# Kernel tuning notes

Measured on AMD Instinct MI355X. Metric: run time of the kernel, lower is better.

Reference implementation:

```python
import jax, jax.numpy as jnp
import numpy as np

VOCAB, E, S, H, L = 32000, 1024, 2048, 16, 2
HS = E // H  # head_size = 64
EPS = 1e-5


def setup_inputs() -> dict:
    key = jax.random.key(0)
    ks = jax.random.split(key, 12)
    sc = 0.02
    inp = {
        "seq": jax.random.randint(ks[0], (S,), 0, VOCAB, dtype=jnp.int64)
        if jax.config.jax_enable_x64 else jax.random.randint(ks[0], (S,), 0, VOCAB, dtype=jnp.int32),
        "tok_emb": jax.random.normal(ks[1], (VOCAB, E), jnp.float32) * sc,
        "pos_emb": jax.random.normal(ks[2], (S, E), jnp.float32) * sc,
        "Wq": jax.random.normal(ks[3], (L, H, E, HS), jnp.float32) * sc,
        "Wk": jax.random.normal(ks[4], (L, H, E, HS), jnp.float32) * sc,
        "Wv": jax.random.normal(ks[5], (L, H, E, HS), jnp.float32) * sc,
        "Wr": jax.random.normal(ks[6], (L, E, E), jnp.float32) * sc,
        "br": jnp.zeros((L, E), jnp.float32),
        "W1": jax.random.normal(ks[7], (L, E, 4 * E), jnp.float32) * sc,
        "b1": jnp.zeros((L, 4 * E), jnp.float32),
        "W2": jax.random.normal(ks[8], (L, 4 * E, E), jnp.float32) * sc,
        "b2": jnp.zeros((L, E), jnp.float32),
        "ln_g": jnp.ones((L, E), jnp.float32),
        "ln_b": jnp.zeros((L, E), jnp.float32),
    }
    return inp


def _layer_norm(x, g, b):
    mu = jnp.mean(x, axis=-1, keepdims=True)
    var = jnp.mean(jnp.square(x - mu), axis=-1, keepdims=True)
    return (x - mu) * jax.lax.rsqrt(var + EPS) * g + b


def reference(seq, tok_emb, pos_emb, Wq, Wk, Wv, Wr, br, W1, b1, W2, b2, ln_g, ln_b):
    # embeddings: [S, E]
    x = tok_emb[seq] + pos_emb
    att_maps = []
    for l in range(L):
        # NOTE: the torch Block reuses the SAME LayerNorm instance twice per block.
        x = _layer_norm(x, ln_g[l], ln_b[l])
        # per-head projections: [H, S, HS]
        q = jnp.einsum('se,hed->hsd', x, Wq[l])
        k = jnp.einsum('se,hed->hsd', x, Wk[l])
        v = jnp.einsum('se,hed->hsd', x, Wv[l])
        # unmasked (encoder) attention, full [H, S, S] scores
        atts = jax.nn.softmax(jnp.einsum('hsd,htd->hst', q, k) / np.sqrt(HS), axis=-1)
        av = jnp.einsum('hst,htd->hsd', atts, v)  # [H, S, HS]
        cat = jnp.transpose(av, (1, 0, 2)).reshape(S, H * HS)  # concat heads -> [S, E]
        x = x + cat @ Wr[l] + br[l]
        x = _layer_norm(x, ln_g[l], ln_b[l])
        x = x + jax.nn.relu(x @ W1[l] + b1[l]) @ W2[l] + b2[l]
        att_maps.append(atts)
    return x, jnp.stack(att_maps)  # ([S,E], [L,H,S,S])
```

## Files before the change

### kernel.cpp

```cpp
#include <hip/hip_runtime.h>
#include <hip/hip_bf16.h>


constexpr int S_ = 2048;
constexpr int E_ = 1024;
constexpr int H_ = 16;
constexpr int HS_ = 64;
constexpr int L_ = 2;
constexpr int FF_ = 4096;

typedef __bf16 bf16;
typedef __bf16 bf16x8 __attribute__((ext_vector_type(8)));
typedef __bf16 bf16x4 __attribute__((ext_vector_type(4)));
typedef float f32x4 __attribute__((ext_vector_type(4)));

__device__ __forceinline__ void gld16(const void* g, const void* l) {
  __builtin_amdgcn_global_load_lds(
      (const __attribute__((address_space(1))) unsigned int*)g,
      (__attribute__((address_space(3))) unsigned int*)l, 16, 0, 0);
}

__global__ __launch_bounds__(256) void embed_ln_k(const int* __restrict__ seq,
                                                  const float* __restrict__ tok,
                                                  const float* __restrict__ pos,
                                                  const float* __restrict__ gw,
                                                  const float* __restrict__ bw,
                                                  float* __restrict__ x,
                                                  bf16* __restrict__ xb) {
  __shared__ float red[8];
  const int row = blockIdx.x, tid = threadIdx.x;
  const int t = seq[row];
  float4 v = ((const float4*)(tok + (long)t * E_))[tid];
  float4 p = ((const float4*)(pos + (long)row * E_))[tid];
  v.x += p.x; v.y += p.y; v.z += p.z; v.w += p.w;
  float s = v.x + v.y + v.z + v.w;
  float ss = v.x * v.x + v.y * v.y + v.z * v.z + v.w * v.w;
  for (int off = 32; off; off >>= 1) {
    s += __shfl_down(s, off);
    ss += __shfl_down(ss, off);
  }
  if ((tid & 63) == 0) { red[(tid >> 6) * 2] = s; red[(tid >> 6) * 2 + 1] = ss; }
  __syncthreads();
  if (tid == 0) {
    float S0 = 0, SS = 0;
    for (int i = 0; i < 4; ++i) { S0 += red[i * 2]; SS += red[i * 2 + 1]; }
    red[0] = S0; red[1] = SS;
  }
  __syncthreads();
  const float mu = red[0] * (1.f / E_);
  const float var = red[1] * (1.f / E_) - mu * mu;
  const float rs = rsqrtf(var + 1e-5f);
  float4 gv = ((const float4*)gw)[tid], bv = ((const float4*)bw)[tid];
  float4 o;
  o.x = (v.x - mu) * rs * gv.x + bv.x;
  o.y = (v.y - mu) * rs * gv.y + bv.y;
  o.z = (v.z - mu) * rs * gv.z + bv.z;
  o.w = (v.w - mu) * rs * gv.w + bv.w;
  ((float4*)(x + (long)row * E_))[tid] = o;
  bf16x4 ob;
  ob[0] = (__bf16)o.x; ob[1] = (__bf16)o.y; ob[2] = (__bf16)o.z; ob[3] = (__bf16)o.w;
  ((bf16x4*)(xb + (long)row * E_))[tid] = ob;
}

__global__ __launch_bounds__(256) void layernorm_k(float* __restrict__ x,
                                                   const float* __restrict__ gw,
                                                   const float* __restrict__ bw,
                                                   bf16* __restrict__ xb) {
  __shared__ float red[8];
  const int row = blockIdx.x, tid = threadIdx.x;
  float4 v = ((const float4*)(x + (long)row * E_))[tid];
  float s = v.x + v.y + v.z + v.w;
  float ss = v.x * v.x + v.y * v.y + v.z * v.z + v.w * v.w;
  for (int off = 32; off; off >>= 1) {
    s += __shfl_down(s, off);
    ss += __shfl_down(ss, off);
  }
  if ((tid & 63) == 0) { red[(tid >> 6) * 2] = s; red[(tid >> 6) * 2 + 1] = ss; }
  __syncthreads();
  if (tid == 0) {
    float S0 = 0, SS = 0;
    for (int i = 0; i < 4; ++i) { S0 += red[i * 2]; SS += red[i * 2 + 1]; }
    red[0] = S0; red[1] = SS;
  }
  __syncthreads();
  const float mu = red[0] * (1.f / E_);
  const float var = red[1] * (1.f / E_) - mu * mu;
  const float rs = rsqrtf(var + 1e-5f);
  float4 gv = ((const float4*)gw)[tid], bv = ((const float4*)bw)[tid];
  float4 o;
  o.x = (v.x - mu) * rs * gv.x + bv.x;
  o.y = (v.y - mu) * rs * gv.y + bv.y;
  o.z = (v.z - mu) * rs * gv.z + bv.z;
  o.w = (v.w - mu) * rs * gv.w + bv.w;
  ((float4*)(x + (long)row * E_))[tid] = o;
  bf16x4 ob;
  ob[0] = (__bf16)o.x; ob[1] = (__bf16)o.y; ob[2] = (__bf16)o.z; ob[3] = (__bf16)o.w;
  ((bf16x4*)(xb + (long)row * E_))[tid] = ob;
}

__global__ __launch_bounds__(256) void repack_k(const float* __restrict__ wq,
                                                const float* __restrict__ wk,
                                                const float* __restrict__ wv,
                                                const float* __restrict__ wr,
                                                const float* __restrict__ w1,
                                                const float* __restrict__ w2,
                                                bf16* __restrict__ qkvT,
                                                bf16* __restrict__ wrT,
                                                bf16* __restrict__ w1T,
                                                bf16* __restrict__ w2T) {
  __shared__ float t[32][33];
  const int tx = threadIdx.x, ty = threadIdx.y;
  const int bid = blockIdx.x;
  const float* src;
  bf16* dst;
  long ld_in, ld_out, r0, c0;
  if (bid < 3072) {
    const int j = bid >> 10;
    const int z = (bid & 1023) >> 6;
    const int rem = bid & 63;
    r0 = (rem >> 1) * 32;
    c0 = (rem & 1) * 32;
    const float* w = j == 0 ? wq : (j == 1 ? wk : wv);
    src = w + (long)z * E_ * HS_;
    dst = qkvT + (long)j * E_ * E_ + (long)z * HS_ * E_;
    ld_in = HS_; ld_out = E_;
  } else if (bid < 4096) {
    const int idx = bid - 3072;
    r0 = (idx >> 5) * 32; c0 = (idx & 31) * 32;
    src = wr; dst = wrT; ld_in = E_; ld_out = E_;
  } else if (bid < 8192) {
    const int idx = bid - 4096;
    r0 = (idx >> 7) * 32; c0 = (idx & 127) * 32;
    src = w1; dst = w1T; ld_in = FF_; ld_out = E_;
  } else {
    const int idx = bid - 8192;
    r0 = (idx >> 5) * 32; c0 = (idx & 31) * 32;
    src = w2; dst = w2T; ld_in = E_; ld_out = FF_;
  }
#pragma unroll
  for (int i = 0; i < 4; ++i)
    t[ty + 8 * i][tx] = src[(r0 + ty + 8 * i) * ld_in + c0 + tx];
  __syncthreads();
#pragma unroll
  for (int i = 0; i < 4; ++i)
    dst[(c0 + ty + 8 * i) * ld_out + r0 + tx] = (__bf16)t[tx][ty + 8 * i];
}

__global__ __launch_bounds__(256) void trans_b2b(const bf16* __restrict__ in,
                                                 bf16* __restrict__ out,
                                                 long ld_in, long ld_out) {
  __shared__ bf16 t[32][33];
  const int tx = threadIdx.x, ty = threadIdx.y;
  const long r0 = (long)blockIdx.x * 32, c0 = (long)blockIdx.y * 32;
#pragma unroll
  for (int i = 0; i < 4; ++i)
    t[ty + 8 * i][tx] = in[(r0 + ty + 8 * i) * ld_in + c0 + tx];
  __syncthreads();
#pragma unroll
  for (int i = 0; i < 4; ++i)
    out[(c0 + ty + 8 * i) * ld_out + r0 + tx] = t[tx][ty + 8 * i];
}

template <int WM, int WN>
__global__ __launch_bounds__(WM * WN * 64) void gemm_lds(
    const bf16* __restrict__ A, const bf16* __restrict__ B,
    long lda, long ldb, int K, int mtiles, float scale,
    const float* __restrict__ bias, const float* __restrict__ resid, int relu,
    float* __restrict__ Cf, long ldc, bf16* __restrict__ Cb, long ldcb) {
  constexpr int BM = WM * 64, BN = WN * 64, NW = WM * WN;
  constexpr int ABYTES = BM * 64;
  constexpr int BUFB = ABYTES + BN * 64;
  constexpr int NCH = BUFB / 1024;
  constexpr int CPT = NCH / NW;
  static_assert(CPT == 4 || CPT == 6, "unexpected CPT");
  __shared__ char smem[3 * BUFB];

  const int tid = threadIdx.x, wid = tid >> 6, lane = tid & 63;
  const int cpx = gridDim.x >> 3;
  const int bid = blockIdx.x;
  const int wg = (bid & 7) * cpx + (bid >> 3);
  const long m0 = (long)(wg % mtiles) * BM;
  const long n0 = (long)(wg / mtiles) * BN;

  const char* gsrc[CPT];
  int ldsbase[CPT];
#pragma unroll
  for (int i = 0; i < CPT; ++i) {
    const int c = wid + i * NW;
    const int s = c * 1024 + lane * 16;
    const bf16* base;
    int kb;
    if (s < ABYTES) {
      const int row = s >> 6;
      kb = (s ^ ((row & 3) << 4)) & 63;
      base = A + (m0 + row) * lda;
    } else {
      const int s2 = s - ABYTES;
      const int row = s2 >> 6;
      kb = (s2 ^ ((row & 3) << 4)) & 63;
      base = B + (n0 + row) * ldb;
    }
    gsrc[i] = (const char*)base + kb;
    ldsbase[i] = c * 1024;
  }

  const int fr = lane & 15, fg = lane >> 4;
  const int wm = wid % WM, wn = wid / WM;
  int aoff[4], boff[4];
#pragma unroll
  for (int t = 0; t < 4; ++t) {
    const int m = wm * 64 + t * 16 + fr;
    aoff[t] = m * 64 + ((16 * fg) ^ ((m & 3) << 4));
    const int n = wn * 64 + t * 16 + fr;
    boff[t] = ABYTES + n * 64 + ((16 * fg) ^ ((n & 3) << 4));
  }

  f32x4 acc[4][4];
#pragma unroll
  for (int i = 0; i < 4; ++i)
#pragma unroll
    for (int j = 0; j < 4; ++j) acc[i][j] = (f32x4){0.f, 0.f, 0.f, 0.f};

  const int nt = K >> 5;

  auto stage = [&](int tile, int buf) {
    const long koff = (long)tile * 64;
#pragma unroll
    for (int i = 0; i < CPT; ++i)
      gld16(gsrc[i] + koff, smem + buf * BUFB + ldsbase[i]);
  };

  stage(0, 0);
  stage(1, 1);

  int cur = 0;
  for (int t = 0; t < nt; ++t) {
    if (t < nt - 1) {
      if constexpr (CPT == 4) asm volatile("s_waitcnt vmcnt(4)" ::: "memory");
      else asm volatile("s_waitcnt vmcnt(6)" ::: "memory");
    } else {
      asm volatile("s_waitcnt vmcnt(0)" ::: "memory");
    }
    __builtin_amdgcn_s_barrier();
    if (t + 2 < nt) {
      int sb = cur + 2; if (sb >= 3) sb -= 3;
      stage(t + 2, sb);
    }
    const char* sbuf = smem + cur * BUFB;
    bf16x8 a[4], b[4];
#pragma unroll
    for (int i = 0; i < 4; ++i) a[i] = *(const bf16x8*)(sbuf + aoff[i]);
#pragma unroll
    for (int i = 0; i < 4; ++i) b[i] = *(const bf16x8*)(sbuf + boff[i]);
#pragma unroll
    for (int i = 0; i < 4; ++i)
#pragma unroll
      for (int j = 0; j < 4; ++j)
        acc[i][j] = __builtin_amdgcn_mfma_f32_16x16x32_bf16(a[i], b[j], acc[i][j], 0, 0, 0);
    cur = cur + 1; if (cur >= 3) cur -= 3;
  }

#pragma unroll
  for (int tm = 0; tm < 4; ++tm) {
#pragma unroll
    for (int tn = 0; tn < 4; ++tn) {
      const long col = n0 + wn * 64 + tn * 16 + fr;
#pragma unroll
      for (int i = 0; i < 4; ++i) {
        const long row = m0 + wm * 64 + tm * 16 + fg * 4 + i;
        float v = acc[tm][tn][i] * scale;
        if (bias) v += bias[col];
        if (relu) v = v > 0.f ? v : 0.f;
        if (resid) v += resid[row * ldc + col];
        if (Cf) Cf[row * ldc + col] = v;
        if (Cb) Cb[row * ldcb + col] = (__bf16)v;
      }
    }
  }
}

__global__ __launch_bounds__(256, 2) void gemm_ksplit(
    const bf16* __restrict__ A, const bf16* __restrict__ B,
    long lda, long ldb, int K, int mtiles, float scale,
    const float* __restrict__ bias, const float* __restrict__ resid, int relu,
    float* __restrict__ Cf, long ldc, bf16* __restrict__ Cb, long ldcb) {
  __shared__ char smem[4 * 16384];

  const int tid = threadIdx.x, w = tid >> 6, lane = tid & 63;
  const int cpx = gridDim.x >> 3;
  const int bid = blockIdx.x;
  const int wg = (bid & 7) * cpx + (bid >> 3);
  const long m0 = (long)(wg % mtiles) * 64;
  const long n0 = (long)(wg / mtiles) * 64;
  const int Kq = K >> 2;
  const long k0w = (long)w * Kq;

  const char* gsrc[8];
  int ldsoff[8];
#pragma unroll
  for (int i = 0; i < 8; ++i) {
    const int s = (i & 3) * 1024 + lane * 16;
    const int row = s >> 6;
    const int kb = (s ^ ((row & 3) << 4)) & 63;
    const bf16* base = (i < 4) ? (A + (m0 + row) * lda + k0w)
                               : (B + (n0 + row) * ldb + k0w);
    gsrc[i] = (const char*)base + kb;
    ldsoff[i] = w * 16384 + i * 1024;
  }

  const int fr = lane & 15, fg = lane >> 4;
  int aoff[4], boff[4];
#pragma unroll
  for (int t = 0; t < 4; ++t) {
    const int m = t * 16 + fr;
    aoff[t] = w * 16384 + m * 64 + ((16 * fg) ^ ((m & 3) << 4));
    boff[t] = aoff[t] + 4096;
  }

  f32x4 acc[4][4];
#pragma unroll
  for (int i = 0; i < 4; ++i)
#pragma unroll
    for (int j = 0; j < 4; ++j) acc[i][j] = (f32x4){0.f, 0.f, 0.f, 0.f};

  const int nt = Kq >> 5;

  auto stage = [&](int tile, int buf) {
    const long koff = (long)tile * 64;
#pragma unroll
    for (int i = 0; i < 8; ++i)
      gld16(gsrc[i] + koff, smem + ldsoff[i] + buf * 8192);
  };

  stage(0, 0);
  if (nt > 1) stage(1, 1);

  for (int t = 0; t < nt; ++t) {
    if (t + 1 < nt) asm volatile("s_waitcnt vmcnt(8)" ::: "memory");
    else asm volatile("s_waitcnt vmcnt(0)" ::: "memory");
    const int bsel = (t & 1) * 8192;
    bf16x8 a[4], b[4];
#pragma unroll
    for (int i = 0; i < 4; ++i) a[i] = *(const bf16x8*)(smem + aoff[i] + bsel);
#pragma unroll
    for (int i = 0; i < 4; ++i) b[i] = *(const bf16x8*)(smem + boff[i] + bsel);
    __builtin_amdgcn_s_setprio(1);
#pragma unroll
    for (int i = 0; i < 4; ++i)
#pragma unroll
      for (int j = 0; j < 4; ++j)
        acc[i][j] = __builtin_amdgcn_mfma_f32_16x16x32_bf16(a[i], b[j], acc[i][j], 0, 0, 0);
    __builtin_amdgcn_s_setprio(0);
    if (t + 2 < nt) stage(t + 2, t & 1);
  }

  __syncthreads();
#pragma unroll
  for (int f = 0; f < 16; ++f)
    *(f32x4*)(smem + w * 16384 + f * 1024 + lane * 16) = acc[f >> 2][f & 3];
  __syncthreads();

#pragma unroll
  for (int tn = 0; tn < 4; ++tn) {
    const int f = w * 4 + tn;
    f32x4 v0 = *(const f32x4*)(smem + 0 * 16384 + f * 1024 + lane * 16);
    f32x4 v1 = *(const f32x4*)(smem + 1 * 16384 + f * 1024 + lane * 16);
    f32x4 v2 = *(const f32x4*)(smem + 2 * 16384 + f * 1024 + lane * 16);
    f32x4 v3 = *(const f32x4*)(smem + 3 * 16384 + f * 1024 + lane * 16);
    f32x4 sv;
#pragma unroll
    for (int i = 0; i < 4; ++i) sv[i] = v0[i] + v1[i] + v2[i] + v3[i];
    const long col = n0 + tn * 16 + fr;
#pragma unroll
    for (int i = 0; i < 4; ++i) {
      const long row = m0 + w * 16 + fg * 4 + i;
      float v = sv[i] * scale;
      if (bias) v += bias[col];
      if (relu) v = v > 0.f ? v : 0.f;
      if (resid) v += resid[row * ldc + col];
      if (Cf) Cf[row * ldc + col] = v;
      if (Cb) Cb[row * ldcb + col] = (__bf16)v;
    }
  }
}

__global__ __launch_bounds__(256, 2) void attn_fused(
    const bf16* __restrict__ qkv,
    const bf16* __restrict__ vt,
    float* __restrict__ att,
    bf16* __restrict__ avb) {
  constexpr int QB = 64, KB = 128;
  constexpr int NKT = S_ / KB;
  constexpr float C2 = 0.1803368801111244f;
  __shared__ char plds[QB * 256];

  const int tid = threadIdx.x, lane = tid & 63, w = tid >> 6;
  const int fr = lane & 15, fg = lane >> 4;
  const int bid = blockIdx.x;
  const int wg = (bid & 7) * 64 + (bid >> 3);
  const int h = wg >> 5;
  const long q0 = (long)(wg & 31) * QB;
  const int q = w * 16 + fr;
  const int swz = (q & 15) << 4;

  bf16x8 qf[2];
#pragma unroll
  for (int k0 = 0; k0 < 2; ++k0)
    qf[k0] = *(const bf16x8*)(qkv + (q0 + q) * (3 * E_) + h * HS_ + k0 * 32 + fg * 8);

  float l_ = 0.f;

  for (int kt = 0; kt < NKT; ++kt) {
    const long t0 = (long)kt * KB;
    bf16x8 kf[8][2];
#pragma unroll
    for (int mt = 0; mt < 8; ++mt)
#pragma unroll
      for (int k0 = 0; k0 < 2; ++k0)
        kf[mt][k0] = *(const bf16x8*)(qkv + (t0 + mt * 16 + fr) * (3 * E_) +
                                      E_ + h * HS_ + k0 * 32 + fg * 8);
    f32x4 acc[8];
#pragma unroll
    for (int mt = 0; mt < 8; ++mt) acc[mt] = (f32x4){0.f, 0.f, 0.f, 0.f};
    __builtin_amdgcn_s_setprio(1);
#pragma unroll
    for (int k0 = 0; k0 < 2; ++k0)
#pragma unroll
      for (int mt = 0; mt < 8; ++mt)
        acc[mt] = __builtin_amdgcn_mfma_f32_16x16x32_bf16(kf[mt][k0], qf[k0], acc[mt], 0, 0, 0);
    __builtin_amdgcn_s_setprio(0);
    float sum = 0.f;
#pragma unroll
    for (int mt = 0; mt < 8; ++mt)
#pragma unroll
      for (int i = 0; i < 4; ++i) sum += __builtin_amdgcn_exp2f(acc[mt][i] * C2);
    l_ += sum;
  }
  l_ += __shfl_xor(l_, 16);
  l_ += __shfl_xor(l_, 32);
  const float li = -__log2f(l_);

  f32x4 ao[4];
#pragma unroll
  for (int d = 0; d < 4; ++d) ao[d] = (f32x4){0.f, 0.f, 0.f, 0.f};

  for (int kt = 0; kt < NKT; ++kt) {
    const long t0 = (long)kt * KB;
    bf16x8 kf[8][2];
#pragma unroll
    for (int mt = 0; mt < 8; ++mt)
#pragma unroll
      for (int k0 = 0; k0 < 2; ++k0)
        kf[mt][k0] = *(const bf16x8*)(qkv + (t0 + mt * 16 + fr) * (3 * E_) +
                                      E_ + h * HS_ + k0 * 32 + fg * 8);
    f32x4 acc[8];
#pragma unroll
    for (int mt = 0; mt < 8; ++mt) acc[mt] = (f32x4){0.f, 0.f, 0.f, 0.f};
    __builtin_amdgcn_s_setprio(1);
#pragma unroll
    for (int k0 = 0; k0 < 2; ++k0)
#pragma unroll
      for (int mt = 0; mt < 8; ++mt)
        acc[mt] = __builtin_amdgcn_mfma_f32_16x16x32_bf16(kf[mt][k0], qf[k0], acc[mt], 0, 0, 0);
    __builtin_amdgcn_s_setprio(0);

    float* arow = att + ((long)h * S_ + q0 + q) * S_ + t0;
#pragma unroll
    for (int mt = 0; mt < 8; ++mt) {
      f32x4 pv;
#pragma unroll
      for (int i = 0; i < 4; ++i)
        pv[i] = __builtin_amdgcn_exp2f(fmaf(acc[mt][i], C2, li));
      __builtin_nontemporal_store(pv, (f32x4*)(arow + mt * 16 + fg * 4));
      bf16x4 pb;
      pb[0] = (__bf16)pv[0]; pb[1] = (__bf16)pv[1];
      pb[2] = (__bf16)pv[2]; pb[3] = (__bf16)pv[3];
      const int tb = (mt * 16 + fg * 4) * 2;
      *(bf16x4*)(plds + q * 256 + ((tb & ~15) ^ swz) + (tb & 15)) = pb;
    }

#pragma unroll
    for (int k0 = 0; k0 < 4; ++k0) {
      const bf16x8 bq = *(const bf16x8*)(plds + q * 256 + ((k0 * 64 + fg * 16) ^ swz));
      __builtin_amdgcn_s_setprio(1);
#pragma unroll
      for (int dmt = 0; dmt < 4; ++dmt) {
        bf16x8 av = *(const bf16x8*)(vt + (long)(h * HS_ + dmt * 16 + fr) * S_ +
                                     t0 + k0 * 32 + fg * 8);
        ao[dmt] = __builtin_amdgcn_mfma_f32_16x16x32_bf16(av, bq, ao[dmt], 0, 0, 0);
      }
      __builtin_amdgcn_s_setprio(0);
    }
  }

#pragma unroll
  for (int dmt = 0; dmt < 4; ++dmt) {
    bf16x4 o;
    o[0] = (__bf16)ao[dmt][0]; o[1] = (__bf16)ao[dmt][1];
    o[2] = (__bf16)ao[dmt][2]; o[3] = (__bf16)ao[dmt][3];
    *(bf16x4*)(avb + (q0 + q) * E_ + h * HS_ + dmt * 16 + fg * 4) = o;
  }
}

extern "C" void kernel_launch(void* const* d_in, const int* in_sizes, int n_in,
                              void* d_out, int out_size, void* d_ws, size_t ws_size,
                              hipStream_t stream) {
  const int* seq = (const int*)d_in[0];
  const float* tok_emb = (const float*)d_in[1];
  const float* pos_emb = (const float*)d_in[2];
  const float* Wq = (const float*)d_in[3];
  const float* Wk = (const float*)d_in[4];
  const float* Wv = (const float*)d_in[5];
  const float* Wr = (const float*)d_in[6];
  const float* br = (const float*)d_in[7];
  const float* W1 = (const float*)d_in[8];
  const float* b1 = (const float*)d_in[9];
  const float* W2 = (const float*)d_in[10];
  const float* b2 = (const float*)d_in[11];
  const float* ln_g = (const float*)d_in[12];
  const float* ln_b = (const float*)d_in[13];

  float* outx = (float*)d_out;
  float* att_all = outx + (long)S_ * E_;

  char* w = (char*)d_ws;
  auto alloc = [&](size_t bytes) {
    char* p = w;
    w += (bytes + 255) & ~(size_t)255;
    return p;
  };
  float* x = (float*)alloc((size_t)S_ * E_ * 4);
  bf16* xb = (bf16*)alloc((size_t)S_ * E_ * 2);
  bf16* qkvb = (bf16*)alloc((size_t)S_ * 3 * E_ * 2);
  bf16* vt = (bf16*)alloc((size_t)E_ * S_ * 2);
  bf16* avb = (bf16*)alloc((size_t)S_ * E_ * 2);
  bf16* hb = (bf16*)alloc((size_t)S_ * FF_ * 2);
  bf16* wqkvT = (bf16*)alloc((size_t)3 * E_ * E_ * 2);
  bf16* wrT = (bf16*)alloc((size_t)E_ * E_ * 2);
  bf16* w1T = (bf16*)alloc((size_t)E_ * FF_ * 2);
  bf16* w2T = (bf16*)alloc((size_t)E_ * FF_ * 2);
  (void)ws_size; (void)in_sizes; (void)n_in; (void)out_size;

  embed_ln_k<<<S_, 256, 0, stream>>>(seq, tok_emb, pos_emb, ln_g, ln_b, x, xb);

  for (int l = 0; l < L_; ++l) {
    repack_k<<<12288, dim3(32, 8, 1), 0, stream>>>(
        Wq + (long)l * H_ * E_ * HS_, Wk + (long)l * H_ * E_ * HS_,
        Wv + (long)l * H_ * E_ * HS_, Wr + (long)l * E_ * E_,
        W1 + (long)l * E_ * FF_, W2 + (long)l * FF_ * E_,
        wqkvT, wrT, w1T, w2T);

    if (l > 0)
      layernorm_k<<<S_, 256, 0, stream>>>(x, ln_g + (long)l * E_, ln_b + (long)l * E_, xb);

    gemm_lds<1, 2><<<768, 128, 0, stream>>>(
        xb, wqkvT, E_, E_, E_, 32, 1.f, nullptr, nullptr, 0,
        nullptr, 0, qkvb, 3 * E_);

    trans_b2b<<<dim3(S_ / 32, E_ / 32, 1), dim3(32, 8, 1), 0, stream>>>(
        qkvb + 2 * E_, vt, 3 * E_, S_);

    float* att_l = att_all + (long)l * H_ * S_ * S_;
    attn_fused<<<512, 256, 0, stream>>>(qkvb, vt, att_l, avb);

    gemm_ksplit<<<32 * 16, 256, 0, stream>>>(
        avb, wrT, E_, E_, E_, 32, 1.f, br + (long)l * E_, x, 0,
        x, E_, nullptr, 0);

    layernorm_k<<<S_, 256, 0, stream>>>(x, ln_g + (long)l * E_, ln_b + (long)l * E_, xb);

    gemm_lds<2, 2><<<dim3(16 * 32), 256, 0, stream>>>(
        xb, w1T, E_, E_, E_, 16, 1.f, b1 + (long)l * FF_, nullptr, 1,
        nullptr, 0, hb, FF_);

    float* xdst = (l == L_ - 1) ? outx : x;
    gemm_ksplit<<<32 * 16, 256, 0, stream>>>(
        hb, w2T, FF_, FF_, FF_, 32, 1.f, b2 + (long)l * E_, x, 0,
        xdst, E_, nullptr, 0);
  }
}
```

Baseline: 691.8 us.

## Fuse V transpose into QKV GEMM epilogue and retile FFN1 GEMM

The QKV projection GEMM now writes the V columns directly into a transposed layout. It stages each output tile through swizzled LDS and stores contiguous rows, which removes the separate trans_b2b kernel launch and its extra read and write of V. V tiles no longer write to qkvb, and the attention kernel only reads V from vt. The FFN1 GEMM also switches from 128x128 tiles with 512 blocks to 64x128 tiles with 1024 blocks of 128 threads, giving more blocks at the cost of less reuse per tile.

```diff
diff --git a/kernel.cpp b/kernel.cpp
--- a/kernel.cpp
+++ b/kernel.cpp
@@ -146,27 +146,13 @@
     dst[(c0 + ty + 8 * i) * ld_out + r0 + tx] = (__bf16)t[tx][ty + 8 * i];
 }
 
-__global__ __launch_bounds__(256) void trans_b2b(const bf16* __restrict__ in,
-                                                 bf16* __restrict__ out,
-                                                 long ld_in, long ld_out) {
-  __shared__ bf16 t[32][33];
-  const int tx = threadIdx.x, ty = threadIdx.y;
-  const long r0 = (long)blockIdx.x * 32, c0 = (long)blockIdx.y * 32;
-#pragma unroll
-  for (int i = 0; i < 4; ++i)
-    t[ty + 8 * i][tx] = in[(r0 + ty + 8 * i) * ld_in + c0 + tx];
-  __syncthreads();
-#pragma unroll
-  for (int i = 0; i < 4; ++i)
-    out[(c0 + ty + 8 * i) * ld_out + r0 + tx] = t[tx][ty + 8 * i];
-}
-
 template <int WM, int WN>
 __global__ __launch_bounds__(WM * WN * 64) void gemm_lds(
     const bf16* __restrict__ A, const bf16* __restrict__ B,
     long lda, long ldb, int K, int mtiles, float scale,
     const float* __restrict__ bias, const float* __restrict__ resid, int relu,
-    float* __restrict__ Cf, long ldc, bf16* __restrict__ Cb, long ldcb) {
+    float* __restrict__ Cf, long ldc, bf16* __restrict__ Cb, long ldcb,
+    bf16* __restrict__ Vt, long vthresh) {
   constexpr int BM = WM * 64, BN = WN * 64, NW = WM * WN;
   constexpr int ABYTES = BM * 64;
   constexpr int BUFB = ABYTES + BN * 64;
@@ -258,6 +244,34 @@
       for (int j = 0; j < 4; ++j)
         acc[i][j] = __builtin_amdgcn_mfma_f32_16x16x32_bf16(a[i], b[j], acc[i][j], 0, 0, 0);
     cur = cur + 1; if (cur >= 3) cur -= 3;
+  }
+
+  if (Vt && n0 >= vthresh) {
+    static_assert(BN * BM * 2 <= 3 * BUFB, "LDS too small for V transpose");
+    __syncthreads();
+#pragma unroll
+    for (int tm = 0; tm < 4; ++tm) {
+#pragma unroll
+      for (int tn = 0; tn < 4; ++tn) {
+        const int col = wn * 64 + tn * 16 + fr;
+        const int rowb = wm * 64 + tm * 16 + fg * 4;
+        bf16x4 o;
+#pragma unroll
+        for (int i = 0; i < 4; ++i) o[i] = (__bf16)(acc[tm][tn][i] * scale);
+        *(bf16x4*)(smem + col * (BM * 2) + ((rowb * 2) ^ ((col & 7) << 4))) = o;
+      }
+    }
+    __syncthreads();
+    constexpr int CHUNKS = BM * 2 / 16;
+    constexpr int COLS_PER_REP = (NW * 64) / CHUNKS;
+    const int k = tid % CHUNKS;
+#pragma unroll
+    for (int rep = 0; rep < BN / COLS_PER_REP; ++rep) {
+      const int col = (tid / CHUNKS) + rep * COLS_PER_REP;
+      bf16x8 v = *(const bf16x8*)(smem + col * (BM * 2) + ((k * 16) ^ ((col & 7) << 4)));
+      *(bf16x8*)(Vt + (n0 - vthresh + col) * (long)S_ + m0 + k * 8) = v;
+    }
+    return;
   }
 
 #pragma unroll
@@ -555,10 +569,7 @@
 
     gemm_lds<1, 2><<<768, 128, 0, stream>>>(
         xb, wqkvT, E_, E_, E_, 32, 1.f, nullptr, nullptr, 0,
-        nullptr, 0, qkvb, 3 * E_);
-
-    trans_b2b<<<dim3(S_ / 32, E_ / 32, 1), dim3(32, 8, 1), 0, stream>>>(
-        qkvb + 2 * E_, vt, 3 * E_, S_);
+        nullptr, 0, qkvb, 3 * E_, vt, 2 * E_);
 
     float* att_l = att_all + (long)l * H_ * S_ * S_;
     attn_fused<<<512, 256, 0, stream>>>(qkvb, vt, att_l, avb);
@@ -569,9 +580,9 @@
 
     layernorm_k<<<S_, 256, 0, stream>>>(x, ln_g + (long)l * E_, ln_b + (long)l * E_, xb);
 
-    gemm_lds<2, 2><<<dim3(16 * 32), 256, 0, stream>>>(
-        xb, w1T, E_, E_, E_, 16, 1.f, b1 + (long)l * FF_, nullptr, 1,
-        nullptr, 0, hb, FF_);
+    gemm_lds<1, 2><<<1024, 128, 0, stream>>>(
+        xb, w1T, E_, E_, E_, 32, 1.f, b1 + (long)l * FF_, nullptr, 1,
+        nullptr, 0, hb, FF_, nullptr, 0x7fffffffL);
 
     float* xdst = (l == L_ - 1) ? outx : x;
     gemm_ksplit<<<32 * 16, 256, 0, stream>>>(
```

Measured after the change: 700.1 us. About the same (+1.2%).

## Overlap weight repacking with embedding and attention kernels via merged grids

Applied to the files above, without the earlier changes.

Merges the layer-0 weight repack into the embedding+LayerNorm launch, and the layer-1 repack into the layer-0 attention launch as extra blocks. A second weight buffer set is used when workspace allows, so layer-1 weights can be converted while layer-0 attention runs. The aim is to hide the memory-bound repack traffic behind other work and drop separate launches. The cost is extra workspace, and attn_repack_k loses the (256,2) launch-bounds hint, which could change register allocation for the attention blocks.

```diff
diff --git a/kernel.cpp b/kernel.cpp
--- a/kernel.cpp
+++ b/kernel.cpp
@@ -20,97 +20,19 @@
       (__attribute__((address_space(3))) unsigned int*)l, 16, 0, 0);
 }
 
-__global__ __launch_bounds__(256) void embed_ln_k(const int* __restrict__ seq,
-                                                  const float* __restrict__ tok,
-                                                  const float* __restrict__ pos,
-                                                  const float* __restrict__ gw,
-                                                  const float* __restrict__ bw,
-                                                  float* __restrict__ x,
-                                                  bf16* __restrict__ xb) {
-  __shared__ float red[8];
-  const int row = blockIdx.x, tid = threadIdx.x;
-  const int t = seq[row];
-  float4 v = ((const float4*)(tok + (long)t * E_))[tid];
-  float4 p = ((const float4*)(pos + (long)row * E_))[tid];
-  v.x += p.x; v.y += p.y; v.z += p.z; v.w += p.w;
-  float s = v.x + v.y + v.z + v.w;
-  float ss = v.x * v.x + v.y * v.y + v.z * v.z + v.w * v.w;
-  for (int off = 32; off; off >>= 1) {
-    s += __shfl_down(s, off);
-    ss += __shfl_down(ss, off);
-  }
-  if ((tid & 63) == 0) { red[(tid >> 6) * 2] = s; red[(tid >> 6) * 2 + 1] = ss; }
-  __syncthreads();
-  if (tid == 0) {
-    float S0 = 0, SS = 0;
-    for (int i = 0; i < 4; ++i) { S0 += red[i * 2]; SS += red[i * 2 + 1]; }
-    red[0] = S0; red[1] = SS;
-  }
-  __syncthreads();
-  const float mu = red[0] * (1.f / E_);
-  const float var = red[1] * (1.f / E_) - mu * mu;
-  const float rs = rsqrtf(var + 1e-5f);
-  float4 gv = ((const float4*)gw)[tid], bv = ((const float4*)bw)[tid];
-  float4 o;
-  o.x = (v.x - mu) * rs * gv.x + bv.x;
-  o.y = (v.y - mu) * rs * gv.y + bv.y;
-  o.z = (v.z - mu) * rs * gv.z + bv.z;
-  o.w = (v.w - mu) * rs * gv.w + bv.w;
-  ((float4*)(x + (long)row * E_))[tid] = o;
-  bf16x4 ob;
-  ob[0] = (__bf16)o.x; ob[1] = (__bf16)o.y; ob[2] = (__bf16)o.z; ob[3] = (__bf16)o.w;
-  ((bf16x4*)(xb + (long)row * E_))[tid] = ob;
-}
-
-__global__ __launch_bounds__(256) void layernorm_k(float* __restrict__ x,
-                                                   const float* __restrict__ gw,
-                                                   const float* __restrict__ bw,
-                                                   bf16* __restrict__ xb) {
-  __shared__ float red[8];
-  const int row = blockIdx.x, tid = threadIdx.x;
-  float4 v = ((const float4*)(x + (long)row * E_))[tid];
-  float s = v.x + v.y + v.z + v.w;
-  float ss = v.x * v.x + v.y * v.y + v.z * v.z + v.w * v.w;
-  for (int off = 32; off; off >>= 1) {
-    s += __shfl_down(s, off);
-    ss += __shfl_down(ss, off);
-  }
-  if ((tid & 63) == 0) { red[(tid >> 6) * 2] = s; red[(tid >> 6) * 2 + 1] = ss; }
-  __syncthreads();
-  if (tid == 0) {
-    float S0 = 0, SS = 0;
-    for (int i = 0; i < 4; ++i) { S0 += red[i * 2]; SS += red[i * 2 + 1]; }
-    red[0] = S0; red[1] = SS;
-  }
-  __syncthreads();
-  const float mu = red[0] * (1.f / E_);
-  const float var = red[1] * (1.f / E_) - mu * mu;
-  const float rs = rsqrtf(var + 1e-5f);
-  float4 gv = ((const float4*)gw)[tid], bv = ((const float4*)bw)[tid];
-  float4 o;
-  o.x = (v.x - mu) * rs * gv.x + bv.x;
-  o.y = (v.y - mu) * rs * gv.y + bv.y;
-  o.z = (v.z - mu) * rs * gv.z + bv.z;
-  o.w = (v.w - mu) * rs * gv.w + bv.w;
-  ((float4*)(x + (long)row * E_))[tid] = o;
-  bf16x4 ob;
-  ob[0] = (__bf16)o.x; ob[1] = (__bf16)o.y; ob[2] = (__bf16)o.z; ob[3] = (__bf16)o.w;
-  ((bf16x4*)(xb + (long)row * E_))[tid] = ob;
-}
-
-__global__ __launch_bounds__(256) void repack_k(const float* __restrict__ wq,
-                                                const float* __restrict__ wk,
-                                                const float* __restrict__ wv,
-                                                const float* __restrict__ wr,
-                                                const float* __restrict__ w1,
-                                                const float* __restrict__ w2,
-                                                bf16* __restrict__ qkvT,
-                                                bf16* __restrict__ wrT,
-                                                bf16* __restrict__ w1T,
-                                                bf16* __restrict__ w2T) {
-  __shared__ float t[32][33];
-  const int tx = threadIdx.x, ty = threadIdx.y;
-  const int bid = blockIdx.x;
+__device__ __forceinline__ void repack_tile(int bid, int tid,
+                                            const float* __restrict__ wq,
+                                            const float* __restrict__ wk,
+                                            const float* __restrict__ wv,
+                                            const float* __restrict__ wr,
+                                            const float* __restrict__ w1,
+                                            const float* __restrict__ w2,
+                                            bf16* __restrict__ qkvT,
+                                            bf16* __restrict__ wrT,
+                                            bf16* __restrict__ w1T,
+                                            bf16* __restrict__ w2T,
+                                            float (*t)[33]) {
+  const int tx = tid & 31, ty = tid >> 5;
   const float* src;
   bf16* dst;
   long ld_in, ld_out, r0, c0;
@@ -146,6 +68,101 @@
     dst[(c0 + ty + 8 * i) * ld_out + r0 + tx] = (__bf16)t[tx][ty + 8 * i];
 }
 
+__global__ __launch_bounds__(256) void embed_ln_repack_k(
+    const int* __restrict__ seq, const float* __restrict__ tok,
+    const float* __restrict__ pos, const float* __restrict__ gw,
+    const float* __restrict__ bw, float* __restrict__ x, bf16* __restrict__ xb,
+    const float* wq, const float* wk, const float* wv, const float* wr,
+    const float* w1, const float* w2,
+    bf16* qkvT, bf16* wrT, bf16* w1T, bf16* w2T) {
+  __shared__ float red[8];
+  __shared__ float t[32][33];
+  const int tid = threadIdx.x;
+  if (blockIdx.x >= S_) {
+    repack_tile(blockIdx.x - S_, tid, wq, wk, wv, wr, w1, w2,
+                qkvT, wrT, w1T, w2T, t);
+    return;
+  }
+  const int row = blockIdx.x;
+  const int tk = seq[row];
+  float4 v = ((const float4*)(tok + (long)tk * E_))[tid];
+  float4 p = ((const float4*)(pos + (long)row * E_))[tid];
+  v.x += p.x; v.y += p.y; v.z += p.z; v.w += p.w;
+  float s = v.x + v.y + v.z + v.w;
+  float ss = v.x * v.x + v.y * v.y + v.z * v.z + v.w * v.w;
+  for (int off = 32; off; off >>= 1) {
+    s += __shfl_down(s, off);
+    ss += __shfl_down(ss, off);
+  }
+  if ((tid & 63) == 0) { red[(tid >> 6) * 2] = s; red[(tid >> 6) * 2 + 1] = ss; }
+  __syncthreads();
+  if (tid == 0) {
+    float S0 = 0, SS = 0;
+    for (int i = 0; i < 4; ++i) { S0 += red[i * 2]; SS += red[i * 2 + 1]; }
+    red[0] = S0; red[1] = SS;
+  }
+  __syncthreads();
+  const float mu = red[0] * (1.f / E_);
+  const float var = red[1] * (1.f / E_) - mu * mu;
+  const float rs = rsqrtf(var + 1e-5f);
+  float4 gv = ((const float4*)gw)[tid], bv = ((const float4*)bw)[tid];
+  float4 o;
+  o.x = (v.x - mu) * rs * gv.x + bv.x;
+  o.y = (v.y - mu) * rs * gv.y + bv.y;
+  o.z = (v.z - mu) * rs * gv.z + bv.z;
+  o.w = (v.w - mu) * rs * gv.w + bv.w;
+  ((float4*)(x + (long)row * E_))[tid] = o;
+  bf16x4 ob;
+  ob[0] = (__bf16)o.x; ob[1] = (__bf16)o.y; ob[2] = (__bf16)o.z; ob[3] = (__bf16)o.w;
+  ((bf16x4*)(xb + (long)row * E_))[tid] = ob;
+}
+
+__global__ __launch_bounds__(256) void layernorm_k(float* __restrict__ x,
+                                                   const float* __restrict__ gw,
+                                                   const float* __restrict__ bw,
+                                                   bf16* __restrict__ xb) {
+  __shared__ float red[8];
+  const int row = blockIdx.x, tid = threadIdx.x;
+  float4 v = ((const float4*)(x + (long)row * E_))[tid];
+  float s = v.x + v.y + v.z + v.w;
+  float ss = v.x * v.x + v.y * v.y + v.z * v.z + v.w * v.w;
+  for (int off = 32; off; off >>= 1) {
+    s += __shfl_down(s, off);
+    ss += __shfl_down(ss, off);
+  }
+  if ((tid & 63) == 0) { red[(tid >> 6) * 2] = s; red[(tid >> 6) * 2 + 1] = ss; }
+  __syncthreads();
+  if (tid == 0) {
+    float S0 = 0, SS = 0;
+    for (int i = 0; i < 4; ++i) { S0 += red[i * 2]; SS += red[i * 2 + 1]; }
+    red[0] = S0; red[1] = SS;
+  }
+  __syncthreads();
+  const float mu = red[0] * (1.f / E_);
+  const float var = red[1] * (1.f / E_) - mu * mu;
+  const float rs = rsqrtf(var + 1e-5f);
+  float4 gv = ((const float4*)gw)[tid], bv = ((const float4*)bw)[tid];
+  float4 o;
+  o.x = (v.x - mu) * rs * gv.x + bv.x;
+  o.y = (v.y - mu) * rs * gv.y + bv.y;
+  o.z = (v.z - mu) * rs * gv.z + bv.z;
+  o.w = (v.w - mu) * rs * gv.w + bv.w;
+  ((float4*)(x + (long)row * E_))[tid] = o;
+  bf16x4 ob;
+  ob[0] = (__bf16)o.x; ob[1] = (__bf16)o.y; ob[2] = (__bf16)o.z; ob[3] = (__bf16)o.w;
+  ((bf16x4*)(xb + (long)row * E_))[tid] = ob;
+}
+
+__global__ __launch_bounds__(256) void repack_k(const float* wq, const float* wk,
+                                                const float* wv, const float* wr,
+                                                const float* w1, const float* w2,
+                                                bf16* qkvT, bf16* wrT,
+                                                bf16* w1T, bf16* w2T) {
+  __shared__ float t[32][33];
+  repack_tile(blockIdx.x, threadIdx.x, wq, wk, wv, wr, w1, w2,
+              qkvT, wrT, w1T, w2T, t);
+}
+
 __global__ __launch_bounds__(256) void trans_b2b(const bf16* __restrict__ in,
                                                  bf16* __restrict__ out,
                                                  long ld_in, long ld_out) {
@@ -384,22 +401,20 @@
   }
 }
 
-__global__ __launch_bounds__(256, 2) void attn_fused(
-    const bf16* __restrict__ qkv,
-    const bf16* __restrict__ vt,
-    float* __restrict__ att,
-    bf16* __restrict__ avb) {
-  constexpr int QB = 64, KB = 128;
+__device__ __forceinline__ void attn_body(int bid, int tid,
+                                          const bf16* __restrict__ qkv,
+                                          const bf16* __restrict__ vt,
+                                          float* __restrict__ att,
+                                          bf16* __restrict__ avb,
+                                          char* plds) {
+  constexpr int KB = 128;
   constexpr int NKT = S_ / KB;
   constexpr float C2 = 0.1803368801111244f;
-  __shared__ char plds[QB * 256];
-
-  const int tid = threadIdx.x, lane = tid & 63, w = tid >> 6;
+  const int lane = tid & 63, w = tid >> 6;
   const int fr = lane & 15, fg = lane >> 4;
-  const int bid = blockIdx.x;
   const int wg = (bid & 7) * 64 + (bid >> 3);
   const int h = wg >> 5;
-  const long q0 = (long)(wg & 31) * QB;
+  const long q0 = (long)(wg & 31) * 64;
   const int q = w * 16 + fr;
   const int swz = (q & 15) << 4;
 
@@ -499,6 +514,29 @@
     o[0] = (__bf16)ao[dmt][0]; o[1] = (__bf16)ao[dmt][1];
     o[2] = (__bf16)ao[dmt][2]; o[3] = (__bf16)ao[dmt][3];
     *(bf16x4*)(avb + (q0 + q) * E_ + h * HS_ + dmt * 16 + fg * 4) = o;
+  }
+}
+
+__global__ __launch_bounds__(256, 2) void attn_fused(
+    const bf16* __restrict__ qkv, const bf16* __restrict__ vt,
+    float* __restrict__ att, bf16* __restrict__ avb) {
+  __shared__ char plds[64 * 256];
+  attn_body(blockIdx.x, threadIdx.x, qkv, vt, att, avb, plds);
+}
+
+__global__ __launch_bounds__(256) void attn_repack_k(
+    const bf16* __restrict__ qkv, const bf16* __restrict__ vt,
+    float* __restrict__ att, bf16* __restrict__ avb,
+    const float* wq, const float* wk, const float* wv, const float* wr,
+    const float* w1, const float* w2,
+    bf16* qkvT, bf16* wrT, bf16* w1T, bf16* w2T) {
+  __shared__ char plds[64 * 256];
+  __shared__ float t[32][33];
+  if (blockIdx.x < 512) {
+    attn_body(blockIdx.x, threadIdx.x, qkv, vt, att, avb, plds);
+  } else {
+    repack_tile(blockIdx.x - 512, threadIdx.x, wq, wk, wv, wr, w1, w2,
+                qkvT, wrT, w1T, w2T, t);
   }
 }
 
@@ -535,47 +573,77 @@
   bf16* vt = (bf16*)alloc((size_t)E_ * S_ * 2);
   bf16* avb = (bf16*)alloc((size_t)S_ * E_ * 2);
   bf16* hb = (bf16*)alloc((size_t)S_ * FF_ * 2);
-  bf16* wqkvT = (bf16*)alloc((size_t)3 * E_ * E_ * 2);
-  bf16* wrT = (bf16*)alloc((size_t)E_ * E_ * 2);
-  bf16* w1T = (bf16*)alloc((size_t)E_ * FF_ * 2);
-  bf16* w2T = (bf16*)alloc((size_t)E_ * FF_ * 2);
-  (void)ws_size; (void)in_sizes; (void)n_in; (void)out_size;
-
-  embed_ln_k<<<S_, 256, 0, stream>>>(seq, tok_emb, pos_emb, ln_g, ln_b, x, xb);
+  bf16* qkvT0 = (bf16*)alloc((size_t)3 * E_ * E_ * 2);
+  bf16* wrT0 = (bf16*)alloc((size_t)E_ * E_ * 2);
+  bf16* w1T0 = (bf16*)alloc((size_t)E_ * FF_ * 2);
+  bf16* w2T0 = (bf16*)alloc((size_t)E_ * FF_ * 2);
+  const size_t wset_bytes =
+      (((size_t)3 * E_ * E_ * 2 + 255) & ~(size_t)255) +
+      (((size_t)E_ * E_ * 2 + 255) & ~(size_t)255) +
+      2 * (((size_t)E_ * FF_ * 2 + 255) & ~(size_t)255);
+  const size_t used = (size_t)(w - (char*)d_ws);
+  const bool dbl = ws_size >= used + wset_bytes;
+  bf16 *qkvT1 = qkvT0, *wrT1 = wrT0, *w1T1 = w1T0, *w2T1 = w2T0;
+  if (dbl) {
+    qkvT1 = (bf16*)alloc((size_t)3 * E_ * E_ * 2);
+    wrT1 = (bf16*)alloc((size_t)E_ * E_ * 2);
+    w1T1 = (bf16*)alloc((size_t)E_ * FF_ * 2);
+    w2T1 = (bf16*)alloc((size_t)E_ * FF_ * 2);
+  }
+  (void)in_sizes; (void)n_in; (void)out_size;
+
+  bf16* qkvT[2] = {qkvT0, qkvT1};
+  bf16* wrT[2] = {wrT0, wrT1};
+  bf16* w1T[2] = {w1T0, w1T1};
+  bf16* w2T[2] = {w2T0, w2T1};
+
+  embed_ln_repack_k<<<S_ + 12288, 256, 0, stream>>>(
+      seq, tok_emb, pos_emb, ln_g, ln_b, x, xb,
+      Wq, Wk, Wv, Wr, W1, W2, qkvT0, wrT0, w1T0, w2T0);
 
   for (int l = 0; l < L_; ++l) {
-    repack_k<<<12288, dim3(32, 8, 1), 0, stream>>>(
-        Wq + (long)l * H_ * E_ * HS_, Wk + (long)l * H_ * E_ * HS_,
-        Wv + (long)l * H_ * E_ * HS_, Wr + (long)l * E_ * E_,
-        W1 + (long)l * E_ * FF_, W2 + (long)l * FF_ * E_,
-        wqkvT, wrT, w1T, w2T);
-
-    if (l > 0)
+    if (l > 0) {
+      if (!dbl)
+        repack_k<<<12288, 256, 0, stream>>>(
+            Wq + (long)l * H_ * E_ * HS_, Wk + (long)l * H_ * E_ * HS_,
+            Wv + (long)l * H_ * E_ * HS_, Wr + (long)l * E_ * E_,
+            W1 + (long)l * E_ * FF_, W2 + (long)l * FF_ * E_,
+            qkvT[1], wrT[1], w1T[1], w2T[1]);
       layernorm_k<<<S_, 256, 0, stream>>>(x, ln_g + (long)l * E_, ln_b + (long)l * E_, xb);
+    }
 
     gemm_lds<1, 2><<<768, 128, 0, stream>>>(
-        xb, wqkvT, E_, E_, E_, 32, 1.f, nullptr, nullptr, 0,
+        xb, qkvT[l], E_, E_, E_, 32, 1.f, nullptr, nullptr, 0,
         nullptr, 0, qkvb, 3 * E_);
 
     trans_b2b<<<dim3(S_ / 32, E_ / 32, 1), dim3(32, 8, 1), 0, stream>>>(
         qkvb + 2 * E_, vt, 3 * E_, S_);
 
     float* att_l = att_all + (long)l * H_ * S_ * S_;
-    attn_fused<<<512, 256, 0, stream>>>(qkvb, vt, att_l, avb);
+    if (l == 0 && dbl) {
+      attn_repack_k<<<512 + 12288, 256, 0, stream>>>(
+          qkvb, vt, att_l, avb,
+          Wq + (long)H_ * E_ * HS_, Wk + (long)H_ * E_ * HS_,
+          Wv + (long)H_ * E_ * HS_, Wr + (long)E_ * E_,
+          W1 + (long)E_ * FF_, W2 + (long)FF_ * E_,
+          qkvT[1], wrT[1], w1T[1], w2T[1]);
+    } else {
+      attn_fused<<<512, 256, 0, stream>>>(qkvb, vt, att_l, avb);
+    }
 
     gemm_ksplit<<<32 * 16, 256, 0, stream>>>(
-        avb, wrT, E_, E_, E_, 32, 1.f, br + (long)l * E_, x, 0,
+        avb, wrT[l], E_, E_, E_, 32, 1.f, br + (long)l * E_, x, 0,
         x, E_, nullptr, 0);
 
     layernorm_k<<<S_, 256, 0, stream>>>(x, ln_g + (long)l * E_, ln_b + (long)l * E_, xb);
 
     gemm_lds<2, 2><<<dim3(16 * 32), 256, 0, stream>>>(
-        xb, w1T, E_, E_, E_, 16, 1.f, b1 + (long)l * FF_, nullptr, 1,
+        xb, w1T[l], E_, E_, E_, 16, 1.f, b1 + (long)l * FF_, nullptr, 1,
         nullptr, 0, hb, FF_);
 
     float* xdst = (l == L_ - 1) ? outx : x;
     gemm_ksplit<<<32 * 16, 256, 0, stream>>>(
-        hb, w2T, FF_, FF_, FF_, 32, 1.f, b2 + (long)l * E_, x, 0,
+        hb, w2T[l], FF_, FF_, FF_, 32, 1.f, b2 + (long)l * E_, x, 0,
         xdst, E_, nullptr, 0);
   }
 }
```

Result: no change. 684.7 us (-1.0%).
